# Kernel optimization log

Measured on AMD Instinct MI355X. Metric: run time of the kernel, lower is better.

The kernel has to match this reference:

```python
import jax, jax.numpy as jnp
import numpy as np

B, S, V, D, H, F, L = 8, 1024, 32000, 1024, 16, 4096, 6
HD = D // H
EPS = 1e-5  # torch LayerNorm default


def _sinusoidal_pe(max_len, d):
    pos = jnp.arange(max_len, dtype=jnp.float32)[:, None]
    div = jnp.power(10000.0, jnp.arange(0, d, 2, dtype=jnp.float32) / d)
    X = pos / div  # [max_len, d/2]
    P = jnp.zeros((max_len, d), dtype=jnp.float32)
    P = P.at[:, 0::2].set(jnp.sin(X))
    P = P.at[:, 1::2].set(jnp.cos(X))
    return P  # [max_len, d]


def setup_inputs() -> dict:
    key = jax.random.key(0)
    ks = jax.random.split(key, 20)
    g = lambda k, shape: (jax.random.normal(k, shape, dtype=jnp.float32) * 0.02)
    inp = {
        'src': jax.random.randint(ks[0], (B, S), 0, V, dtype=jnp.int32),
        'src_mask': jnp.ones((B, 1, 1, S), dtype=jnp.int32),
        'emb': g(ks[1], (V, D)),
        'Wq': g(ks[2], (L, D, D)), 'bq': jnp.zeros((L, D)),
        'Wk': g(ks[3], (L, D, D)), 'bk': jnp.zeros((L, D)),
        'Wv': g(ks[4], (L, D, D)), 'bv': jnp.zeros((L, D)),
        'Wo': g(ks[5], (L, D, D)), 'bo': jnp.zeros((L, D)),
        'ln1_g': jnp.ones((L, D)), 'ln1_b': jnp.zeros((L, D)),
        'W1': g(ks[6], (L, D, F)), 'b1': jnp.zeros((L, F)),
        'W2': g(ks[7], (L, F, D)), 'b2': jnp.zeros((L, D)),
        'ln2_g': jnp.ones((L, D)), 'ln2_b': jnp.zeros((L, D)),
    }
    return inp


def _layernorm(x, g, b):
    mu = jnp.mean(x, axis=-1, keepdims=True)
    var = jnp.mean(jnp.square(x - mu), axis=-1, keepdims=True)
    return (x - mu) * jax.lax.rsqrt(var + EPS) * g + b


def _encoder(src, src_mask, emb, Wq, bq, Wk, bk, Wv, bv, Wo, bo,
             ln1_g, ln1_b, W1, b1, W2, b2, ln2_g, ln2_b):
    x = emb[src] * jnp.sqrt(jnp.float32(D))            # [B,S,D]
    x = x + _sinusoidal_pe(S, D)[None, :, :]            # absolute PE
    neg = jnp.float32(-1e10)
    mask0 = (src_mask == 0)

    def layer(x, p):
        (wq, bq_, wk, bk_, wv, bv_, wo, bo_, g1, b1n, w1, b1_, w2, b2_, g2, b2n) = p
        q = (x @ wq + bq_).reshape(B, S, H, HD)
        k = (x @ wk + bk_).reshape(B, S, H, HD)
        v = (x @ wv + bv_).reshape(B, S, H, HD)
        energy = jnp.einsum('bqhd,bkhd->bhqk', q, k) / jnp.sqrt(jnp.float32(HD))
        energy = jnp.where(mask0, neg, energy)
        attn = jax.nn.softmax(energy, axis=-1)
        ctx = jnp.einsum('bhqk,bkhd->bqhd', attn, v).reshape(B, S, D)
        x = _layernorm(x + (ctx @ wo + bo_), g1, b1n)
        ff = jax.nn.relu(x @ w1 + b1_) @ w2 + b2_
        x = _layernorm(x + ff, g2, b2n)
        return x, None

    params = (Wq, bq, Wk, bk, Wv, bv, Wo, bo, ln1_g, ln1_b, W1, b1, W2, b2, ln2_g, ln2_b)
    x, _ = jax.lax.scan(layer, x, params)
    return x


def reference(src, src_mask, emb, Wq, bq, Wk, bk, Wv, bv, Wo, bo,
              ln1_g, ln1_b, W1, b1, W2, b2, ln2_g, ln2_b):
    return _encoder(src, src_mask, emb, Wq, bq, Wk, bk, Wv, bv, Wo, bo,
                    ln1_g, ln1_b, W1, b1, W2, b2, ln2_g, ln2_b)
```

## Files before the change

kernel.cpp:

```cpp
#include <hip/hip_runtime.h>
#include <hip/hip_bf16.h>
#include <math.h>

#define BB 8
#define SS 1024
#define DD 1024
#define HH 16
#define HDIM 64
#define FFD 4096
#define LL 6
#define MM (BB*SS)

typedef unsigned short u16;
typedef __bf16 bf16x8 __attribute__((ext_vector_type(8)));
typedef float f32x4 __attribute__((ext_vector_type(4)));

__device__ __forceinline__ u16 f2b(float f) {
    union { float f; unsigned u; } x; x.f = f;
    unsigned r = x.u + 0x7fffu + ((x.u >> 16) & 1u);
    return (u16)(r >> 16);
}

__device__ __forceinline__ f32x4 mfma16(bf16x8 a, bf16x8 b, f32x4 c) {
    return __builtin_amdgcn_mfma_f32_16x16x32_bf16(a, b, c, 0, 0, 0);
}

__device__ __forceinline__ void async16(const u16* g, char* lds) {
    __builtin_amdgcn_global_load_lds(
        (const __attribute__((address_space(1))) void*)g,
        (__attribute__((address_space(3))) void*)lds, 16, 0, 0);
}

__global__ __launch_bounds__(256) void embed_pe_kernel(
        const int* __restrict__ src, const float* __restrict__ emb,
        float* __restrict__ xout, u16* __restrict__ xb) {
    int row = blockIdx.x;
    int s = row & (SS - 1);
    int tok = src[row];
    int c0 = threadIdx.x * 4;
    const float4 e = *(const float4*)(emb + (size_t)tok * DD + c0);
    float o[4] = {e.x, e.y, e.z, e.w};
    #pragma unroll
    for (int i = 0; i < 4; ++i) {
        int c = c0 + i;
        int j = c & ~1;
        float div = powf(10000.0f, (float)j / (float)DD);
        float arg = (float)s / div;
        float pe = (c & 1) ? cosf(arg) : sinf(arg);
        o[i] = o[i] * 32.0f + pe;
    }
    float4 ov = {o[0], o[1], o[2], o[3]};
    *(float4*)(xout + (size_t)row * DD + c0) = ov;
    u16 pk[4] = {f2b(o[0]), f2b(o[1]), f2b(o[2]), f2b(o[3])};
    uint2 pv; __builtin_memcpy(&pv, pk, 8);
    *(uint2*)(xb + (size_t)row * DD + c0) = pv;
}

__global__ __launch_bounds__(256) void transpose_cvt_kernel(
        const float* __restrict__ in, u16* __restrict__ out, int R, int C) {
    __shared__ float tile[32][33];
    int c0 = blockIdx.x * 32, r0 = blockIdx.y * 32;
    int tx = threadIdx.x & 31, ty = threadIdx.x >> 5;
    #pragma unroll
    for (int i = 0; i < 4; ++i) {
        int r = ty + i * 8;
        tile[r][tx] = in[(size_t)(r0 + r) * C + c0 + tx];
    }
    __syncthreads();
    #pragma unroll
    for (int i = 0; i < 4; ++i) {
        int rr = ty + i * 8;
        out[(size_t)(c0 + rr) * R + r0 + tx] = f2b(tile[tx][rr]);
    }
}

template <int MODE>
__global__ __launch_bounds__(256) void gemm_bt(
        const u16* __restrict__ A, const u16* __restrict__ Bt,
        const float* __restrict__ bias, void* __restrict__ Cp,
        int M, int N, int K) {
    __shared__ __align__(16) u16 Al[2][128 * 32];
    __shared__ __align__(16) u16 Bl[2][128 * 32];
    int t = threadIdx.x;
    int w = t >> 6, lane = t & 63, lg = lane >> 4, lr = lane & 15;
    int wr = w >> 1, wc = w & 1;
    int row0 = blockIdx.y * 128, col0 = blockIdx.x * 128;

    f32x4 acc[4][4];
    #pragma unroll
    for (int m = 0; m < 4; ++m)
        #pragma unroll
        for (int n = 0; n < 4; ++n) acc[m][n] = (f32x4){0.f, 0.f, 0.f, 0.f};

    const u16* ag = A + (size_t)(row0 + (t >> 2)) * K + (t & 3) * 8;
    const u16* bg = Bt + (size_t)(col0 + (t >> 2)) * K + (t & 3) * 8;

    auto stage = [&](int buf, int k0) {
        char* adst = (char*)(&Al[buf][0]) + w * 1024;
        char* bdst = (char*)(&Bl[buf][0]) + w * 1024;
        async16(ag + k0, adst);
        async16(ag + (size_t)64 * K + k0, adst + 4096);
        async16(bg + k0, bdst);
        async16(bg + (size_t)64 * K + k0, bdst + 4096);
    };

    stage(0, 0);
    int nt = K >> 5;
    for (int kt = 0; kt < nt; ++kt) {
        __syncthreads();
        int cur = kt & 1;
        if (kt + 1 < nt) stage(cur ^ 1, (kt + 1) << 5);
        bf16x8 af[4], bf[4];
        #pragma unroll
        for (int m = 0; m < 4; ++m)
            af[m] = *(const bf16x8*)&Al[cur][(wr * 64 + m * 16 + lr) * 32 + lg * 8];
        #pragma unroll
        for (int n = 0; n < 4; ++n)
            bf[n] = *(const bf16x8*)&Bl[cur][(wc * 64 + n * 16 + lr) * 32 + lg * 8];
        #pragma unroll
        for (int m = 0; m < 4; ++m)
            #pragma unroll
            for (int n = 0; n < 4; ++n)
                acc[m][n] = mfma16(af[m], bf[n], acc[m][n]);
    }

    float* Cf = (float*)Cp;
    u16* Cb = (u16*)Cp;
    #pragma unroll
    for (int n = 0; n < 4; ++n) {
        int col = col0 + wc * 64 + n * 16 + lr;
        float bn = bias[col];
        #pragma unroll
        for (int m = 0; m < 4; ++m) {
            int rowb = row0 + wr * 64 + m * 16 + lg * 4;
            f32x4 a = acc[m][n];
            if (MODE == 3) {
                u16 pk[4];
                #pragma unroll
                for (int r = 0; r < 4; ++r) pk[r] = f2b(a[r] + bn);
                int b = rowb >> 10, s = rowb & (SS - 1);
                int hh = col >> 6, d = col & (HDIM - 1);
                uint2 pv; __builtin_memcpy(&pv, pk, 8);
                *(uint2*)(Cb + (size_t)((b * HH + hh) * HDIM + d) * SS + s) = pv;
            } else {
                #pragma unroll
                for (int r = 0; r < 4; ++r) {
                    float val = a[r] + bn;
                    size_t idx = (size_t)(rowb + r) * N + col;
                    if (MODE == 0) Cf[idx] = val;
                    else if (MODE == 1) Cb[idx] = f2b(val);
                    else Cb[idx] = f2b(fmaxf(val, 0.0f));
                }
            }
        }
    }
}

__global__ __launch_bounds__(256) void attn_kernel(
        const u16* __restrict__ q, const u16* __restrict__ k,
        const u16* __restrict__ vt, const int* __restrict__ mask,
        u16* __restrict__ ctx) {
    __shared__ __align__(16) u16 plds[4][16][72];
    int w = threadIdx.x >> 6, lane = threadIdx.x & 63;
    int lg = lane >> 4, lr = lane & 15;
    int qt = blockIdx.x, bh = blockIdx.y;
    int b = bh >> 4, h = bh & 15;
    int q0 = qt * 64 + w * 16;

    const u16* qbase = q + (size_t)(b * SS + q0 + lr) * DD + h * HDIM + lg * 8;
    bf16x8 qf0 = *(const bf16x8*)qbase;
    bf16x8 qf1 = *(const bf16x8*)(qbase + 32);

    float mrun[4], ssum[4];
    f32x4 acc[4];
    #pragma unroll
    for (int r = 0; r < 4; ++r) { mrun[r] = -1e30f; ssum[r] = 0.f; }
    #pragma unroll
    for (int n = 0; n < 4; ++n) acc[n] = (f32x4){0.f, 0.f, 0.f, 0.f};
    u16 (*pl)[72] = plds[w];

    for (int k0 = 0; k0 < SS; k0 += 64) {
        f32x4 sc[4];
        #pragma unroll
        for (int f = 0; f < 4; ++f) {
            const u16* kb = k + (size_t)(b * SS + k0 + f * 16 + lr) * DD + h * HDIM + lg * 8;
            bf16x8 kf0 = *(const bf16x8*)kb;
            bf16x8 kf1 = *(const bf16x8*)(kb + 32);
            f32x4 z = (f32x4){0.f, 0.f, 0.f, 0.f};
            z = mfma16(qf0, kf0, z);
            z = mfma16(qf1, kf1, z);
            sc[f] = z;
        }
        float sv[4][4];
        #pragma unroll
        for (int f = 0; f < 4; ++f) {
            bool msk = (mask[b * SS + k0 + f * 16 + lr] == 0);
            #pragma unroll
            for (int r = 0; r < 4; ++r)
                sv[f][r] = msk ? -1e10f : sc[f][r] * 0.125f;
        }
        float mn[4], al[4], ls[4];
        #pragma unroll
        for (int r = 0; r < 4; ++r) {
            float v = fmaxf(fmaxf(sv[0][r], sv[1][r]), fmaxf(sv[2][r], sv[3][r]));
            v = fmaxf(v, __shfl_xor(v, 1));
            v = fmaxf(v, __shfl_xor(v, 2));
            v = fmaxf(v, __shfl_xor(v, 4));
            v = fmaxf(v, __shfl_xor(v, 8));
            mn[r] = fmaxf(mrun[r], v);
            al[r] = __expf(mrun[r] - mn[r]);
            mrun[r] = mn[r];
            ls[r] = 0.f;
        }
        #pragma unroll
        for (int f = 0; f < 4; ++f)
            #pragma unroll
            for (int r = 0; r < 4; ++r) {
                float p = __expf(sv[f][r] - mn[r]);
                ls[r] += p;
                pl[lg * 4 + r][f * 16 + lr] = f2b(p);
            }
        #pragma unroll
        for (int r = 0; r < 4; ++r) {
            float v = ls[r];
            v += __shfl_xor(v, 1); v += __shfl_xor(v, 2);
            v += __shfl_xor(v, 4); v += __shfl_xor(v, 8);
            ssum[r] = ssum[r] * al[r] + v;
        }
        #pragma unroll
        for (int n = 0; n < 4; ++n)
            #pragma unroll
            for (int r = 0; r < 4; ++r) acc[n][r] *= al[r];
        #pragma unroll
        for (int c = 0; c < 2; ++c) {
            bf16x8 pf = *(const bf16x8*)&pl[lr][c * 32 + lg * 8];
            #pragma unroll
            for (int n = 0; n < 4; ++n) {
                const u16* vb = vt + (size_t)(bh * HDIM + n * 16 + lr) * SS + k0 + c * 32 + lg * 8;
                bf16x8 vf = *(const bf16x8*)vb;
                acc[n] = mfma16(pf, vf, acc[n]);
            }
        }
    }
    #pragma unroll
    for (int n = 0; n < 4; ++n)
        #pragma unroll
        for (int r = 0; r < 4; ++r) {
            float o = acc[n][r] / ssum[r];
            ctx[(size_t)(b * SS + q0 + lg * 4 + r) * DD + h * HDIM + n * 16 + lr] = f2b(o);
        }
}

__global__ __launch_bounds__(256) void ln_kernel(
        float* __restrict__ x, const float* __restrict__ proj,
        const float* __restrict__ g, const float* __restrict__ bb,
        u16* __restrict__ xb) {
    int row = blockIdx.x, t = threadIdx.x;
    size_t base = (size_t)row * DD + t * 4;
    float4 xv = *(const float4*)(x + base);
    float4 pv = *(const float4*)(proj + base);
    float r0 = xv.x + pv.x, r1 = xv.y + pv.y, r2 = xv.z + pv.z, r3 = xv.w + pv.w;
    float s1 = r0 + r1 + r2 + r3;
    float s2 = r0 * r0 + r1 * r1 + r2 * r2 + r3 * r3;
    #pragma unroll
    for (int off = 1; off < 64; off <<= 1) {
        s1 += __shfl_xor(s1, off);
        s2 += __shfl_xor(s2, off);
    }
    __shared__ float a1[4], a2[4];
    int w = t >> 6, lane = t & 63;
    if (lane == 0) { a1[w] = s1; a2[w] = s2; }
    __syncthreads();
    s1 = a1[0] + a1[1] + a1[2] + a1[3];
    s2 = a2[0] + a2[1] + a2[2] + a2[3];
    float mu = s1 * (1.0f / DD);
    float var = s2 * (1.0f / DD) - mu * mu;
    float rs = rsqrtf(var + 1e-5f);
    float4 gv = *(const float4*)(g + t * 4);
    float4 bv = *(const float4*)(bb + t * 4);
    float o0 = (r0 - mu) * rs * gv.x + bv.x;
    float o1 = (r1 - mu) * rs * gv.y + bv.y;
    float o2 = (r2 - mu) * rs * gv.z + bv.z;
    float o3 = (r3 - mu) * rs * gv.w + bv.w;
    float4 ov = {o0, o1, o2, o3};
    *(float4*)(x + base) = ov;
    u16 pk[4] = {f2b(o0), f2b(o1), f2b(o2), f2b(o3)};
    uint2 pv2; __builtin_memcpy(&pv2, pk, 8);
    *(uint2*)(xb + base) = pv2;
}

extern "C" void kernel_launch(void* const* d_in, const int* in_sizes, int n_in,
                              void* d_out, int out_size, void* d_ws, size_t ws_size,
                              hipStream_t stream) {
    const int*   src  = (const int*)d_in[0];
    const int*   mask = (const int*)d_in[1];
    const float* emb  = (const float*)d_in[2];
    const float* Wq   = (const float*)d_in[3];
    const float* bq   = (const float*)d_in[4];
    const float* Wk   = (const float*)d_in[5];
    const float* bk   = (const float*)d_in[6];
    const float* Wv   = (const float*)d_in[7];
    const float* bv   = (const float*)d_in[8];
    const float* Wo   = (const float*)d_in[9];
    const float* bo   = (const float*)d_in[10];
    const float* g1   = (const float*)d_in[11];
    const float* be1  = (const float*)d_in[12];
    const float* W1   = (const float*)d_in[13];
    const float* b1   = (const float*)d_in[14];
    const float* W2   = (const float*)d_in[15];
    const float* b2   = (const float*)d_in[16];
    const float* g2   = (const float*)d_in[17];
    const float* be2  = (const float*)d_in[18];
    (void)in_sizes; (void)n_in; (void)out_size; (void)ws_size;

    float* x = (float*)d_out;
    char* ws = (char*)d_ws;
    const size_t MiB = 1024 * 1024;
    u16* xb   = (u16*)(ws + 0);
    u16* qb   = (u16*)(ws + 16 * MiB);
    u16* kb   = (u16*)(ws + 32 * MiB);
    u16* vtb  = (u16*)(ws + 48 * MiB);
    u16* ctx  = (u16*)(ws + 64 * MiB);
    u16* ffh  = (u16*)(ws + 16 * MiB);
    float* proj = (float*)(ws + 80 * MiB);
    u16* wqT  = (u16*)(ws + 112 * MiB);
    u16* wkT  = (u16*)(ws + 114 * MiB);
    u16* wvT  = (u16*)(ws + 116 * MiB);
    u16* woT  = (u16*)(ws + 118 * MiB);
    u16* w1T  = (u16*)(ws + 120 * MiB);
    u16* w2T  = (u16*)(ws + 128 * MiB);

    embed_pe_kernel<<<MM, 256, 0, stream>>>(src, emb, x, xb);

    for (int l = 0; l < LL; ++l) {
        transpose_cvt_kernel<<<dim3(32, 32), 256, 0, stream>>>(Wq + (size_t)l * DD * DD, wqT, DD, DD);
        transpose_cvt_kernel<<<dim3(32, 32), 256, 0, stream>>>(Wk + (size_t)l * DD * DD, wkT, DD, DD);
        transpose_cvt_kernel<<<dim3(32, 32), 256, 0, stream>>>(Wv + (size_t)l * DD * DD, wvT, DD, DD);
        transpose_cvt_kernel<<<dim3(32, 32), 256, 0, stream>>>(Wo + (size_t)l * DD * DD, woT, DD, DD);
        transpose_cvt_kernel<<<dim3(128, 32), 256, 0, stream>>>(W1 + (size_t)l * DD * FFD, w1T, DD, FFD);
        transpose_cvt_kernel<<<dim3(32, 128), 256, 0, stream>>>(W2 + (size_t)l * FFD * DD, w2T, FFD, DD);

        gemm_bt<1><<<dim3(8, 64), 256, 0, stream>>>(xb, wqT, bq + l * DD, qb, MM, DD, DD);
        gemm_bt<1><<<dim3(8, 64), 256, 0, stream>>>(xb, wkT, bk + l * DD, kb, MM, DD, DD);
        gemm_bt<3><<<dim3(8, 64), 256, 0, stream>>>(xb, wvT, bv + l * DD, vtb, MM, DD, DD);
        attn_kernel<<<dim3(16, 128), 256, 0, stream>>>(qb, kb, vtb, mask, ctx);
        gemm_bt<0><<<dim3(8, 64), 256, 0, stream>>>(ctx, woT, bo + l * DD, proj, MM, DD, DD);
        ln_kernel<<<MM, 256, 0, stream>>>(x, proj, g1 + l * DD, be1 + l * DD, xb);
        gemm_bt<2><<<dim3(32, 64), 256, 0, stream>>>(xb, w1T, b1 + l * FFD, ffh, MM, FFD, DD);
        gemm_bt<0><<<dim3(8, 64), 256, 0, stream>>>(ffh, w2T, b2 + l * DD, proj, MM, DD, FFD);
        ln_kernel<<<MM, 256, 0, stream>>>(x, proj, g2 + l * DD, be2 + l * DD, xb);
    }
}
```

Before: 3.846 ms.

## Process two query tiles per wave in attention and prefetch K registers

The attention kernel now has each wave handle 32 query rows (two 16-row tiles) instead of 16, so every K and V fragment loaded from global memory is reused across two MFMA tiles. K fragments for the next 64-key block are double-buffered in registers and prefetched, and V fragments are loaded ahead of the softmax work. The grid is halved to match. The aim is less redundant K/V global traffic and hidden load latency, at the cost of higher register pressure, possibly lower occupancy, and fewer blocks.

```diff
diff --git a/kernel.cpp b/kernel.cpp
--- a/kernel.cpp
+++ b/kernel.cpp
@@ -160,95 +160,142 @@
         const u16* __restrict__ q, const u16* __restrict__ k,
         const u16* __restrict__ vt, const int* __restrict__ mask,
         u16* __restrict__ ctx) {
-    __shared__ __align__(16) u16 plds[4][16][72];
+    __shared__ __align__(16) u16 plds[4][2][16][72];
     int w = threadIdx.x >> 6, lane = threadIdx.x & 63;
     int lg = lane >> 4, lr = lane & 15;
     int qt = blockIdx.x, bh = blockIdx.y;
     int b = bh >> 4, h = bh & 15;
-    int q0 = qt * 64 + w * 16;
-
-    const u16* qbase = q + (size_t)(b * SS + q0 + lr) * DD + h * HDIM + lg * 8;
-    bf16x8 qf0 = *(const bf16x8*)qbase;
-    bf16x8 qf1 = *(const bf16x8*)(qbase + 32);
-
-    float mrun[4], ssum[4];
-    f32x4 acc[4];
-    #pragma unroll
-    for (int r = 0; r < 4; ++r) { mrun[r] = -1e30f; ssum[r] = 0.f; }
-    #pragma unroll
-    for (int n = 0; n < 4; ++n) acc[n] = (f32x4){0.f, 0.f, 0.f, 0.f};
-    u16 (*pl)[72] = plds[w];
-
-    for (int k0 = 0; k0 < SS; k0 += 64) {
-        f32x4 sc[4];
+    int q0 = qt * 128 + w * 32;
+
+    bf16x8 qf[2][2];
+    #pragma unroll
+    for (int m = 0; m < 2; ++m) {
+        const u16* qb = q + (size_t)(b * SS + q0 + m * 16 + lr) * DD + h * HDIM + lg * 8;
+        qf[m][0] = *(const bf16x8*)qb;
+        qf[m][1] = *(const bf16x8*)(qb + 32);
+    }
+
+    float mrun[2][4], ssum[2][4];
+    f32x4 acc[2][4];
+    #pragma unroll
+    for (int m = 0; m < 2; ++m) {
+        #pragma unroll
+        for (int r = 0; r < 4; ++r) { mrun[m][r] = -1e30f; ssum[m][r] = 0.f; }
+        #pragma unroll
+        for (int n = 0; n < 4; ++n) acc[m][n] = (f32x4){0.f, 0.f, 0.f, 0.f};
+    }
+
+    const u16* kbase = k + (size_t)(b * SS + lr) * DD + h * HDIM + lg * 8;
+    const u16* vbase = vt + (size_t)(bh * HDIM + lr) * SS + lg * 8;
+    const int* mbase = mask + b * SS + lr;
+
+    auto loadK = [&](bf16x8 (&kr)[4][2], int k0) {
         #pragma unroll
         for (int f = 0; f < 4; ++f) {
-            const u16* kb = k + (size_t)(b * SS + k0 + f * 16 + lr) * DD + h * HDIM + lg * 8;
-            bf16x8 kf0 = *(const bf16x8*)kb;
-            bf16x8 kf1 = *(const bf16x8*)(kb + 32);
-            f32x4 z = (f32x4){0.f, 0.f, 0.f, 0.f};
-            z = mfma16(qf0, kf0, z);
-            z = mfma16(qf1, kf1, z);
-            sc[f] = z;
+            const u16* p = kbase + (size_t)(k0 + f * 16) * DD;
+            kr[f][0] = *(const bf16x8*)p;
+            kr[f][1] = *(const bf16x8*)(p + 32);
         }
-        float sv[4][4];
-        #pragma unroll
-        for (int f = 0; f < 4; ++f) {
-            bool msk = (mask[b * SS + k0 + f * 16 + lr] == 0);
-            #pragma unroll
-            for (int r = 0; r < 4; ++r)
-                sv[f][r] = msk ? -1e10f : sc[f][r] * 0.125f;
+    };
+
+    auto step = [&](bf16x8 (&kc)[4][2], bf16x8 (&kn)[4][2], int t, bool pre) {
+        int k0 = t * 64;
+        if (pre) loadK(kn, k0 + 64);
+        f32x4 sc[2][4];
+        #pragma unroll
+        for (int m = 0; m < 2; ++m)
+            #pragma unroll
+            for (int f = 0; f < 4; ++f) {
+                f32x4 z = (f32x4){0.f, 0.f, 0.f, 0.f};
+                z = mfma16(qf[m][0], kc[f][0], z);
+                z = mfma16(qf[m][1], kc[f][1], z);
+                sc[m][f] = z;
+            }
+        bf16x8 vr[4][2];
+        #pragma unroll
+        for (int n = 0; n < 4; ++n)
+            #pragma unroll
+            for (int c = 0; c < 2; ++c)
+                vr[n][c] = *(const bf16x8*)(vbase + (size_t)(n * 16) * SS + k0 + c * 32);
+        int mk[4];
+        #pragma unroll
+        for (int f = 0; f < 4; ++f) mk[f] = mbase[k0 + f * 16];
+        #pragma unroll
+        for (int m = 0; m < 2; ++m) {
+            float sv[4][4];
+            #pragma unroll
+            for (int f = 0; f < 4; ++f) {
+                bool msk = (mk[f] == 0);
+                #pragma unroll
+                for (int r = 0; r < 4; ++r)
+                    sv[f][r] = msk ? -1e10f : sc[m][f][r] * 0.125f;
+            }
+            float mn[4], al[4], ls[4];
+            #pragma unroll
+            for (int r = 0; r < 4; ++r) {
+                float v = fmaxf(fmaxf(sv[0][r], sv[1][r]), fmaxf(sv[2][r], sv[3][r]));
+                v = fmaxf(v, __shfl_xor(v, 1));
+                v = fmaxf(v, __shfl_xor(v, 2));
+                v = fmaxf(v, __shfl_xor(v, 4));
+                v = fmaxf(v, __shfl_xor(v, 8));
+                mn[r] = fmaxf(mrun[m][r], v);
+                al[r] = __expf(mrun[m][r] - mn[r]);
+                mrun[m][r] = mn[r];
+                ls[r] = 0.f;
+            }
+            #pragma unroll
+            for (int f = 0; f < 4; ++f)
+                #pragma unroll
+                for (int r = 0; r < 4; ++r) {
+                    float p = __expf(sv[f][r] - mn[r]);
+                    ls[r] += p;
+                    plds[w][m][lg * 4 + r][f * 16 + lr] = f2b(p);
+                }
+            #pragma unroll
+            for (int r = 0; r < 4; ++r) {
+                float v = ls[r];
+                v += __shfl_xor(v, 1); v += __shfl_xor(v, 2);
+                v += __shfl_xor(v, 4); v += __shfl_xor(v, 8);
+                ssum[m][r] = ssum[m][r] * al[r] + v;
+            }
+            #pragma unroll
+            for (int n = 0; n < 4; ++n)
+                #pragma unroll
+                for (int r = 0; r < 4; ++r) acc[m][n][r] *= al[r];
         }
-        float mn[4], al[4], ls[4];
-        #pragma unroll
-        for (int r = 0; r < 4; ++r) {
-            float v = fmaxf(fmaxf(sv[0][r], sv[1][r]), fmaxf(sv[2][r], sv[3][r]));
-            v = fmaxf(v, __shfl_xor(v, 1));
-            v = fmaxf(v, __shfl_xor(v, 2));
-            v = fmaxf(v, __shfl_xor(v, 4));
-            v = fmaxf(v, __shfl_xor(v, 8));
-            mn[r] = fmaxf(mrun[r], v);
-            al[r] = __expf(mrun[r] - mn[r]);
-            mrun[r] = mn[r];
-            ls[r] = 0.f;
-        }
-        #pragma unroll
-        for (int f = 0; f < 4; ++f)
+        #pragma unroll
+        for (int m = 0; m < 2; ++m)
+            #pragma unroll
+            for (int c = 0; c < 2; ++c) {
+                bf16x8 pf = *(const bf16x8*)&plds[w][m][lr][c * 32 + lg * 8];
+                #pragma unroll
+                for (int n = 0; n < 4; ++n)
+                    acc[m][n] = mfma16(pf, vr[n][c], acc[m][n]);
+            }
+    };
+
+    bf16x8 kA[4][2], kB[4][2];
+    loadK(kA, 0);
+    for (int tt = 0; tt < 7; ++tt) {
+        step(kA, kB, 2 * tt, true);
+        step(kB, kA, 2 * tt + 1, true);
+    }
+    step(kA, kB, 14, true);
+    step(kB, kA, 15, false);
+
+    #pragma unroll
+    for (int m = 0; m < 2; ++m) {
+        float rin[4];
+        #pragma unroll
+        for (int r = 0; r < 4; ++r) rin[r] = 1.0f / ssum[m][r];
+        #pragma unroll
+        for (int n = 0; n < 4; ++n)
             #pragma unroll
             for (int r = 0; r < 4; ++r) {
-                float p = __expf(sv[f][r] - mn[r]);
-                ls[r] += p;
-                pl[lg * 4 + r][f * 16 + lr] = f2b(p);
-            }
-        #pragma unroll
-        for (int r = 0; r < 4; ++r) {
-            float v = ls[r];
-            v += __shfl_xor(v, 1); v += __shfl_xor(v, 2);
-            v += __shfl_xor(v, 4); v += __shfl_xor(v, 8);
-            ssum[r] = ssum[r] * al[r] + v;
-        }
-        #pragma unroll
-        for (int n = 0; n < 4; ++n)
-            #pragma unroll
-            for (int r = 0; r < 4; ++r) acc[n][r] *= al[r];
-        #pragma unroll
-        for (int c = 0; c < 2; ++c) {
-            bf16x8 pf = *(const bf16x8*)&pl[lr][c * 32 + lg * 8];
-            #pragma unroll
-            for (int n = 0; n < 4; ++n) {
-                const u16* vb = vt + (size_t)(bh * HDIM + n * 16 + lr) * SS + k0 + c * 32 + lg * 8;
-                bf16x8 vf = *(const bf16x8*)vb;
-                acc[n] = mfma16(pf, vf, acc[n]);
-            }
-        }
-    }
-    #pragma unroll
-    for (int n = 0; n < 4; ++n)
-        #pragma unroll
-        for (int r = 0; r < 4; ++r) {
-            float o = acc[n][r] / ssum[r];
-            ctx[(size_t)(b * SS + q0 + lg * 4 + r) * DD + h * HDIM + n * 16 + lr] = f2b(o);
-        }
+                float o = acc[m][n][r] * rin[r];
+                ctx[(size_t)(b * SS + q0 + m * 16 + lg * 4 + r) * DD + h * HDIM + n * 16 + lr] = f2b(o);
+            }
+    }
 }
 
 __global__ __launch_bounds__(256) void ln_kernel(
@@ -343,7 +390,7 @@
         gemm_bt<1><<<dim3(8, 64), 256, 0, stream>>>(xb, wqT, bq + l * DD, qb, MM, DD, DD);
         gemm_bt<1><<<dim3(8, 64), 256, 0, stream>>>(xb, wkT, bk + l * DD, kb, MM, DD, DD);
         gemm_bt<3><<<dim3(8, 64), 256, 0, stream>>>(xb, wvT, bv + l * DD, vtb, MM, DD, DD);
-        attn_kernel<<<dim3(16, 128), 256, 0, stream>>>(qb, kb, vtb, mask, ctx);
+        attn_kernel<<<dim3(8, 128), 256, 0, stream>>>(qb, kb, vtb, mask, ctx);
         gemm_bt<0><<<dim3(8, 64), 256, 0, stream>>>(ctx, woT, bo + l * DD, proj, MM, DD, DD);
         ln_kernel<<<MM, 256, 0, stream>>>(x, proj, g1 + l * DD, be1 + l * DD, xb);
         gemm_bt<2><<<dim3(32, 64), 256, 0, stream>>>(xb, w1T, b1 + l * FFD, ffh, MM, FFD, DD);
```

Result: no change. 3.787 ms (-1.5%).
